# Kernel tuning notes

Measured on AMD Instinct MI355X. Metric: run time of the kernel, lower is better.

The kernel has to match this reference:

```python
import jax, jax.numpy as jnp
import numpy as np

B, T, I, H, O = 64, 512, 128, 1024, 128
ALPHA = 0.2


def setup_inputs() -> dict:
    key = jax.random.key(0)
    ks = jax.random.split(key, 7)
    inv_sqrt_h = 1.0 / np.sqrt(H)
    return {
        "x": jax.random.normal(ks[0], (B, T, I), dtype=jnp.float32),
        "wi": jax.random.normal(ks[1], (I, H), dtype=jnp.float32) / np.sqrt(I),
        "wrec": jax.random.normal(ks[2], (H, H), dtype=jnp.float32) * inv_sqrt_h,
        "wout": jax.random.normal(ks[3], (H, O), dtype=jnp.float32) * inv_sqrt_h,
        "b": jax.random.normal(ks[4], (H, 1), dtype=jnp.float32) * 0.1,
        "g": jax.random.normal(ks[5], (H, 1), dtype=jnp.float32) * 0.5 + 1.0,
        "h0": jax.random.normal(ks[6], (H,), dtype=jnp.float32) * 0.1,
    }


def reference(x, wi, wrec, wout, b, g, h0):
    # Leaky tanh RNN: h_{t+1} = h_t + alpha*(-h_t + (g*r_t) @ wrec^T + x_t @ wi)
    #                 r_t = tanh(h_t + b); out_t = (g*r_t) @ wout
    gv = g[:, 0]  # (H,)
    bv = b[:, 0]  # (H,)
    batch = x.shape[0]

    r0 = jnp.tanh(h0 + bv)                     # (H,)
    out0 = (gv * r0) @ wout                    # (O,) broadcast over batch

    h_init = jnp.broadcast_to(h0, (batch, h0.shape[0]))
    r_init = jnp.broadcast_to(r0, (batch, h0.shape[0]))

    # precompute input projection for all steps used in the loop (steps 0..T-2)
    xs = jnp.swapaxes(x[:, :-1, :], 0, 1)      # (T-1, B, I)

    def step(carry, x_t):
        h, r = carry
        h = h + ALPHA * (-h + (gv * r) @ wrec.T + x_t @ wi)
        r = jnp.tanh(h + bv)
        out = (gv * r) @ wout                  # (B, O)
        return (h, r), out

    _, outs = jax.lax.scan(step, (h_init, r_init), xs)   # (T-1, B, O)
    outs = jnp.swapaxes(outs, 0, 1)                      # (B, T-1, O)
    out0b = jnp.broadcast_to(out0, (batch, 1, wout.shape[1]))
    return jnp.concatenate([out0b, outs], axis=1)        # (B, T, O)
```

## Files before the change

### kernel.cpp

```cpp
#include <hip/hip_runtime.h>

#define H 1024
#define I_DIM 128
#define O_DIM 128
#define T_DIM 512
#define ALPHA 0.2f
#define NWG 64
#define GSZ 16

typedef short short8 __attribute__((ext_vector_type(8)));
typedef float f32x4 __attribute__((ext_vector_type(4)));

__device__ __forceinline__ unsigned short f2b(float f) {
    union { float f; unsigned u; } x; x.f = f;
    unsigned u = x.u;
    return (unsigned short)((u + 0x7FFFu + ((u >> 16) & 1u)) >> 16);
}
__device__ __forceinline__ float tanh_fast(float x) {
    float e = __expf(2.0f * x);
    return 1.0f - 2.0f * __builtin_amdgcn_rcpf(e + 1.0f);
}
__device__ __forceinline__ short8 ld8f(const float* __restrict__ p) {
    const float4 a = *(const float4*)p;
    const float4 b = *(const float4*)(p + 4);
    short8 r;
    r[0]=(short)f2b(a.x); r[1]=(short)f2b(a.y); r[2]=(short)f2b(a.z); r[3]=(short)f2b(a.w);
    r[4]=(short)f2b(b.x); r[5]=(short)f2b(b.y); r[6]=(short)f2b(b.z); r[7]=(short)f2b(b.w);
    return r;
}
__device__ __forceinline__ void async16(const unsigned short* g, unsigned short* l) {
    __builtin_amdgcn_global_load_lds(
        (const __attribute__((address_space(1))) unsigned int*)(const void*)g,
        (__attribute__((address_space(3))) unsigned int*)(void*)l, 16, 0, 0);
}

__global__ __launch_bounds__(256, 1) void rnn_kernel(
    const float* __restrict__ x, const float* __restrict__ wi,
    const float* __restrict__ wrec, const float* __restrict__ wout,
    const float* __restrict__ bb, const float* __restrict__ gg,
    const float* __restrict__ h0p, float* __restrict__ out,
    unsigned short* __restrict__ aG, unsigned int* __restrict__ bar)
{
    __shared__ unsigned short abuf[32 * 512];
    __shared__ unsigned short aloc[1024];
    __shared__ float opart[4 * 128];

    const int tid  = threadIdx.x;
    const int w    = tid >> 6, lane = tid & 63;
    const int n    = lane & 15, q = lane >> 4;
    const int grp  = blockIdx.x & 3;
    const int ji   = blockIdx.x >> 2;
    const int j0   = ji * 64;
    const int j    = j0 + w * 16 + n;
    const int b0   = grp * 16;
    unsigned int* gbar = bar + grp * 64;

    short8 wfr[32];
#pragma unroll
    for (int kt = 0; kt < 32; ++kt)
        wfr[kt] = ld8f(&wrec[(size_t)j * H + kt * 32 + q * 8]);

    short8 wifr[4];
#pragma unroll
    for (int kt = 0; kt < 4; ++kt) {
        short8 v;
#pragma unroll
        for (int i = 0; i < 8; ++i)
            v[i] = (short)f2b(wi[(size_t)(kt * 32 + q * 8 + i) * H + j]);
        wifr[kt] = v;
    }
    short8 wofr[8];
#pragma unroll
    for (int kk = 0; kk < 8; ++kk) {
        short8 v;
        const int kb = (w * 8 + kk) * 32 + q * 8;
#pragma unroll
        for (int i = 0; i < 8; ++i)
            v[i] = (n < 8) ? (short)f2b(wout[(size_t)(kb + i) * O_DIM + ji * 8 + n]) : (short)0;
        wofr[kk] = v;
    }

    const float gv = gg[j], bv = bb[j], h00 = h0p[j];
    float hreg[4];
#pragma unroll
    for (int r = 0; r < 4; ++r) hreg[r] = h00;

    const int kl    = w * 16 + n;
    const int off_l = (kl >> 5) * 512 + ((kl & 31) >> 3) * 128 + (kl & 7);

    auto do_out = [&](int t) {
        f32x4 oa = {0.f, 0.f, 0.f, 0.f};
#pragma unroll
        for (int kk = 0; kk < 8; ++kk) {
            short8 af = *(const short8*)&abuf[(w * 8 + kk) * 512 + lane * 8];
            oa = __builtin_amdgcn_mfma_f32_16x16x32_bf16(af, wofr[kk], oa, 0, 0, 0);
        }
        if (n < 8) {
#pragma unroll
            for (int r = 0; r < 4; ++r) opart[w * 128 + (4 * q + r) * 8 + n] = oa[r];
        }
        __syncthreads();
        if (tid < 128) {
            float s = opart[tid] + opart[128 + tid] + opart[256 + tid] + opart[384 + tid];
            const int m = tid >> 3, c = tid & 7;
            out[((size_t)(b0 + m) * T_DIM + t) * O_DIM + ji * 8 + c] = s;
        }
    };

    {
        unsigned short a0 = f2b(gv * tanh_fast(h00 + bv));
        unsigned short* d0 = aG + (size_t)grp * 16384 + ji * 1024;
#pragma unroll
        for (int r = 0; r < 4; ++r) d0[off_l + (4 * q + r) * 8] = a0;
    }
    __syncthreads();
    if (tid == 0) __hip_atomic_fetch_add(gbar, 1u, __ATOMIC_RELEASE, __HIP_MEMORY_SCOPE_AGENT);

    short8 xfr[4];
#pragma unroll
    for (int kt = 0; kt < 4; ++kt)
        xfr[kt] = ld8f(&x[(size_t)(b0 + n) * T_DIM * I_DIM + kt * 32 + q * 8]);

    for (int t = 1; t < T_DIM; ++t) {
        f32x4 acc0 = {0.f,0.f,0.f,0.f}, acc1 = {0.f,0.f,0.f,0.f};
        acc0 = __builtin_amdgcn_mfma_f32_16x16x32_bf16(xfr[0], wifr[0], acc0, 0,0,0);
        acc1 = __builtin_amdgcn_mfma_f32_16x16x32_bf16(xfr[1], wifr[1], acc1, 0,0,0);
        acc0 = __builtin_amdgcn_mfma_f32_16x16x32_bf16(xfr[2], wifr[2], acc0, 0,0,0);
        acc1 = __builtin_amdgcn_mfma_f32_16x16x32_bf16(xfr[3], wifr[3], acc1, 0,0,0);

        if (tid == 0) {
            const unsigned target = (unsigned)GSZ * (unsigned)t;
            while (__hip_atomic_load(gbar, __ATOMIC_ACQUIRE, __HIP_MEMORY_SCOPE_AGENT) < target)
                __builtin_amdgcn_s_sleep(1);
        }
        __syncthreads();

        const unsigned short* src = aG + ((size_t)((t - 1) & 1) * 4 + grp) * 16384;
#pragma unroll
        for (int c = 0; c < 8; ++c) {
            const int chunk = w * 8 + c;
            async16(src + chunk * 512 + lane * 8, abuf + chunk * 512);
        }
        __syncthreads();

#pragma unroll
        for (int kt = 0; kt < 32; kt += 2) {
            short8 a0f = *(const short8*)&abuf[kt * 512 + lane * 8];
            short8 a1f = *(const short8*)&abuf[(kt + 1) * 512 + lane * 8];
            acc0 = __builtin_amdgcn_mfma_f32_16x16x32_bf16(a0f, wfr[kt],     acc0, 0,0,0);
            acc1 = __builtin_amdgcn_mfma_f32_16x16x32_bf16(a1f, wfr[kt + 1], acc1, 0,0,0);
        }

#pragma unroll
        for (int r = 0; r < 4; ++r) {
            float z  = acc0[r] + acc1[r];
            float hv = (1.0f - ALPHA) * hreg[r] + ALPHA * z;
            hreg[r] = hv;
            aloc[off_l + (4 * q + r) * 8] = f2b(gv * tanh_fast(hv + bv));
        }
        __syncthreads();

        unsigned short* dst = aG + ((size_t)(t & 1) * 4 + grp) * 16384 + ji * 1024;
        if (tid < 128) *(short8*)(dst + tid * 8) = *(const short8*)&aloc[tid * 8];
        __syncthreads();
        if (tid == 0) __hip_atomic_fetch_add(gbar, 1u, __ATOMIC_RELEASE, __HIP_MEMORY_SCOPE_AGENT);

        do_out(t - 1);

        if (t < T_DIM - 1) {
#pragma unroll
            for (int kt = 0; kt < 4; ++kt)
                xfr[kt] = ld8f(&x[((size_t)(b0 + n) * T_DIM + t) * I_DIM + kt * 32 + q * 8]);
        }
    }

    if (tid == 0) {
        const unsigned target = (unsigned)GSZ * (unsigned)T_DIM;
        while (__hip_atomic_load(gbar, __ATOMIC_ACQUIRE, __HIP_MEMORY_SCOPE_AGENT) < target)
            __builtin_amdgcn_s_sleep(1);
    }
    __syncthreads();
    const unsigned short* src = aG + ((size_t)((T_DIM - 1) & 1) * 4 + grp) * 16384;
#pragma unroll
    for (int c = 0; c < 8; ++c) {
        const int chunk = w * 8 + c;
        async16(src + chunk * 512 + lane * 8, abuf + chunk * 512);
    }
    __syncthreads();
    do_out(T_DIM - 1);
}

extern "C" void kernel_launch(void* const* d_in, const int* in_sizes, int n_in,
                              void* d_out, int out_size, void* d_ws, size_t ws_size,
                              hipStream_t stream) {
    const float* x    = (const float*)d_in[0];
    const float* wi   = (const float*)d_in[1];
    const float* wrec = (const float*)d_in[2];
    const float* wout = (const float*)d_in[3];
    const float* bb   = (const float*)d_in[4];
    const float* gg   = (const float*)d_in[5];
    const float* h0   = (const float*)d_in[6];
    float* outp = (float*)d_out;

    unsigned short* aG = (unsigned short*)d_ws;
    unsigned int* bar  = (unsigned int*)((char*)d_ws + 2 * 4 * 16384 * 2);

    hipMemsetAsync(bar, 0, 1024, stream);
    hipLaunchKernelGGL(rnn_kernel, dim3(NWG), dim3(256), 0, stream,
                       x, wi, wrec, wout, bb, gg, h0, outp, aG, bar);
}
```

Before: 2.121 ms.

## Replace group counter barrier with per-wave tag flags for activation exchange

Each wave now publishes its own 256-element slice of the new activations straight from LDS to global memory. It then sets a per-wave tag word with the step number, replacing the workgroup-wide copy, two __syncthreads and the single-thread atomic counter increment. Consumers poll all 64 tags of their group in parallel, one per lane, using a wave vote. The output projection is also moved after the next x load. The aim is to shorten the critical path of the per-step cross-workgroup barrier, at the cost of more polling traffic and relaxed-ordering subtleties.

```diff
diff --git a/kernel.cpp b/kernel.cpp
--- a/kernel.cpp
+++ b/kernel.cpp
@@ -10,6 +10,7 @@
 
 typedef short short8 __attribute__((ext_vector_type(8)));
 typedef float f32x4 __attribute__((ext_vector_type(4)));
+typedef unsigned long long ull_alias __attribute__((may_alias));
 
 __device__ __forceinline__ unsigned short f2b(float f) {
     union { float f; unsigned u; } x; x.f = f;
@@ -39,7 +40,7 @@
     const float* __restrict__ wrec, const float* __restrict__ wout,
     const float* __restrict__ bb, const float* __restrict__ gg,
     const float* __restrict__ h0p, float* __restrict__ out,
-    unsigned short* __restrict__ aG, unsigned int* __restrict__ bar)
+    unsigned short* __restrict__ aG, unsigned int* __restrict__ tagG)
 {
     __shared__ unsigned short abuf[32 * 512];
     __shared__ unsigned short aloc[1024];
@@ -53,7 +54,7 @@
     const int j0   = ji * 64;
     const int j    = j0 + w * 16 + n;
     const int b0   = grp * 16;
-    unsigned int* gbar = bar + grp * 64;
+    unsigned int* tg = tagG + grp * 128;
 
     short8 wfr[32];
 #pragma unroll
@@ -87,6 +88,19 @@
 
     const int kl    = w * 16 + n;
     const int off_l = (kl >> 5) * 512 + ((kl & 31) >> 3) * 128 + (kl & 7);
+    const int slot  = ji * 4 + w;
+
+    auto publish = [&](int t) {
+        asm volatile("" ::: "memory");
+        unsigned long long v = *(const ull_alias*)&aloc[w * 256 + lane * 4];
+        unsigned long long* dst = (unsigned long long*)
+            (aG + (size_t)((t & 1) * 4 + grp) * 16384 + ji * 1024 + w * 256 + lane * 4);
+        __hip_atomic_store(dst, v, __ATOMIC_RELAXED, __HIP_MEMORY_SCOPE_AGENT);
+        asm volatile("s_waitcnt vmcnt(0)" ::: "memory");
+        if (lane == 0)
+            __hip_atomic_store(&tg[(t & 1) * 64 + slot], (unsigned)t,
+                               __ATOMIC_RELAXED, __HIP_MEMORY_SCOPE_AGENT);
+    };
 
     auto do_out = [&](int t) {
         f32x4 oa = {0.f, 0.f, 0.f, 0.f};
@@ -107,14 +121,23 @@
         }
     };
 
+    auto wait_tags = [&](int tv) {
+        const unsigned int* tp = tg + (tv & 1) * 64;
+        for (;;) {
+            unsigned v = __hip_atomic_load(&tp[lane], __ATOMIC_RELAXED,
+                                           __HIP_MEMORY_SCOPE_AGENT);
+            if (__all(v == (unsigned)tv)) break;
+            __builtin_amdgcn_s_sleep(1);
+        }
+        (void)__hip_atomic_load(&tp[0], __ATOMIC_ACQUIRE, __HIP_MEMORY_SCOPE_AGENT);
+    };
+
     {
         unsigned short a0 = f2b(gv * tanh_fast(h00 + bv));
-        unsigned short* d0 = aG + (size_t)grp * 16384 + ji * 1024;
-#pragma unroll
-        for (int r = 0; r < 4; ++r) d0[off_l + (4 * q + r) * 8] = a0;
-    }
-    __syncthreads();
-    if (tid == 0) __hip_atomic_fetch_add(gbar, 1u, __ATOMIC_RELEASE, __HIP_MEMORY_SCOPE_AGENT);
+#pragma unroll
+        for (int r = 0; r < 4; ++r) aloc[off_l + (4 * q + r) * 8] = a0;
+        publish(0);
+    }
 
     short8 xfr[4];
 #pragma unroll
@@ -128,14 +151,10 @@
         acc0 = __builtin_amdgcn_mfma_f32_16x16x32_bf16(xfr[2], wifr[2], acc0, 0,0,0);
         acc1 = __builtin_amdgcn_mfma_f32_16x16x32_bf16(xfr[3], wifr[3], acc1, 0,0,0);
 
-        if (tid == 0) {
-            const unsigned target = (unsigned)GSZ * (unsigned)t;
-            while (__hip_atomic_load(gbar, __ATOMIC_ACQUIRE, __HIP_MEMORY_SCOPE_AGENT) < target)
-                __builtin_amdgcn_s_sleep(1);
-        }
         __syncthreads();
-
-        const unsigned short* src = aG + ((size_t)((t - 1) & 1) * 4 + grp) * 16384;
+        wait_tags(t - 1);
+
+        const unsigned short* src = aG + (size_t)(((t - 1) & 1) * 4 + grp) * 16384;
 #pragma unroll
         for (int c = 0; c < 8; ++c) {
             const int chunk = w * 8 + c;
@@ -158,29 +177,19 @@
             hreg[r] = hv;
             aloc[off_l + (4 * q + r) * 8] = f2b(gv * tanh_fast(hv + bv));
         }
-        __syncthreads();
-
-        unsigned short* dst = aG + ((size_t)(t & 1) * 4 + grp) * 16384 + ji * 1024;
-        if (tid < 128) *(short8*)(dst + tid * 8) = *(const short8*)&aloc[tid * 8];
-        __syncthreads();
-        if (tid == 0) __hip_atomic_fetch_add(gbar, 1u, __ATOMIC_RELEASE, __HIP_MEMORY_SCOPE_AGENT);
-
-        do_out(t - 1);
+        publish(t);
 
         if (t < T_DIM - 1) {
 #pragma unroll
             for (int kt = 0; kt < 4; ++kt)
                 xfr[kt] = ld8f(&x[((size_t)(b0 + n) * T_DIM + t) * I_DIM + kt * 32 + q * 8]);
         }
-    }
-
-    if (tid == 0) {
-        const unsigned target = (unsigned)GSZ * (unsigned)T_DIM;
-        while (__hip_atomic_load(gbar, __ATOMIC_ACQUIRE, __HIP_MEMORY_SCOPE_AGENT) < target)
-            __builtin_amdgcn_s_sleep(1);
-    }
+        do_out(t - 1);
+    }
+
     __syncthreads();
-    const unsigned short* src = aG + ((size_t)((T_DIM - 1) & 1) * 4 + grp) * 16384;
+    wait_tags(T_DIM - 1);
+    const unsigned short* src = aG + (size_t)(((T_DIM - 1) & 1) * 4 + grp) * 16384;
 #pragma unroll
     for (int c = 0; c < 8; ++c) {
         const int chunk = w * 8 + c;
@@ -203,9 +212,9 @@
     float* outp = (float*)d_out;
 
     unsigned short* aG = (unsigned short*)d_ws;
-    unsigned int* bar  = (unsigned int*)((char*)d_ws + 2 * 4 * 16384 * 2);
-
-    hipMemsetAsync(bar, 0, 1024, stream);
+    unsigned int* tagG = (unsigned int*)((char*)d_ws + 2 * 4 * 16384 * 2);
+
+    hipMemsetAsync(tagG, 0xFF, 4 * 2 * 64 * sizeof(unsigned int), stream);
     hipLaunchKernelGGL(rnn_kernel, dim3(NWG), dim3(256), 0, stream,
-                       x, wi, wrec, wout, bb, gg, h0, outp, aG, bar);
-}
+                       x, wi, wrec, wout, bb, gg, h0, outp, aG, tagG);
+}
```

Result: slower. 2.743 ms (+29.3%).
